# Kernel tuning notes

Hardware: AMD Instinct MI355X
Metric: run time of the kernel (lower is better)

Reference implementation:

```python
import jax, jax.numpy as jnp
import numpy as np

LEVELS = [(64, 64), (32, 32), (16, 16), (8, 8)]  # (H, W) per feature level
B, C, NH, NL, NP, NLAYERS, FFN = 8, 256, 8, 4, 4, 6, 1024
Q = sum(h * w for h, w in LEVELS)  # 5440
DH = C // NH


def setup_inputs() -> dict:
    key = jax.random.key(0)
    ks = iter(jax.random.split(key, 40))
    def rn(shape, s=0.02):
        return jax.random.normal(next(ks), shape, dtype=jnp.float32) * s
    return {
        'src_flat': jax.random.normal(next(ks), (B, Q, C), dtype=jnp.float32),
        'pos_flat': jax.random.normal(next(ks), (B, Q, C), dtype=jnp.float32) * 0.1,
        'level_embed': rn((NL, C), 0.1),
        'W_samp': rn((NLAYERS, C, NH * NL * NP * 2)),
        'b_samp': rn((NLAYERS, NH * NL * NP * 2), 0.1),
        'W_attn': rn((NLAYERS, C, NH * NL * NP)),
        'b_attn': rn((NLAYERS, NH * NL * NP), 0.1),
        'W_val': rn((NLAYERS, C, C)),
        'b_val': jnp.zeros((NLAYERS, C), jnp.float32),
        'W_out': rn((NLAYERS, C, C)),
        'b_out': jnp.zeros((NLAYERS, C), jnp.float32),
        'g1': jnp.ones((NLAYERS, C), jnp.float32),
        'b1': jnp.zeros((NLAYERS, C), jnp.float32),
        'W_fc1': rn((NLAYERS, C, FFN)),
        'b_fc1': jnp.zeros((NLAYERS, FFN), jnp.float32),
        'W_fc2': rn((NLAYERS, FFN, C)),
        'b_fc2': jnp.zeros((NLAYERS, C), jnp.float32),
        'g2': jnp.ones((NLAYERS, C), jnp.float32),
        'b2': jnp.zeros((NLAYERS, C), jnp.float32),
    }


def layer_norm(x, g, b):
    m = x.mean(-1, keepdims=True)
    v = ((x - m) ** 2).mean(-1, keepdims=True)
    return (x - m) * jax.lax.rsqrt(v + 1e-5) * g + b


def get_reference_points():
    # valid_ratios are all ones (masks are all-False), so ref pts are identical per level dim
    pts = []
    for (h, w) in LEVELS:
        ry = (jnp.arange(h, dtype=jnp.float32) + 0.5) / h
        rx = (jnp.arange(w, dtype=jnp.float32) + 0.5) / w
        yy, xx = jnp.meshgrid(ry, rx, indexing='ij')
        pts.append(jnp.stack([xx.ravel(), yy.ravel()], -1))
    return jnp.concatenate(pts, 0)  # [Q, 2] in (x, y)


def ms_deform_attn(query, src, ref_pts, Ws, bs, Wa, ba, Wv, bv, Wo, bo):
    value = (src @ Wv + bv).reshape(B, Q, NH, DH)
    off = (query @ Ws + bs).reshape(B, Q, NH, NL, NP, 2)
    aw = jax.nn.softmax((query @ Wa + ba).reshape(B, Q, NH, NL * NP), axis=-1)
    aw = aw.reshape(B, Q, NH, NL, NP).transpose(0, 2, 1, 3, 4)  # [B,NH,Q,NL,NP]
    normalizer = jnp.array([[w, h] for (h, w) in LEVELS], jnp.float32)  # (x, y) per level
    loc = ref_pts[None, :, None, None, None, :] + off / normalizer[None, None, None, :, None, :]
    out = jnp.zeros((B, NH, Q, DH), jnp.float32)
    start = 0
    for l, (h, w) in enumerate(LEVELS):
        v_l = value[:, start:start + h * w].transpose(0, 2, 1, 3)  # [B,NH,HW,DH]
        start += h * w
        loc_l = loc[:, :, :, l]  # [B,Q,NH,NP,2]
        x = loc_l[..., 0] * w - 0.5  # grid_sample align_corners=False pixel coords
        y = loc_l[..., 1] * h - 0.5
        x0 = jnp.floor(x)
        y0 = jnp.floor(y)
        fx = x - x0
        fy = y - y0
        sampled = jnp.zeros((B, NH, Q, NP, DH), jnp.float32)
        for dy, dx in ((0, 0), (0, 1), (1, 0), (1, 1)):
            cy = y0 + dy
            cx = x0 + dx
            wgt = (fy if dy else 1.0 - fy) * (fx if dx else 1.0 - fx)
            valid = (cy >= 0) & (cy < h) & (cx >= 0) & (cx < w)  # zero padding
            wgt = jnp.where(valid, wgt, 0.0)
            idx = (jnp.clip(cy, 0, h - 1) * w + jnp.clip(cx, 0, w - 1)).astype(jnp.int32)
            idx = idx.transpose(0, 2, 1, 3).reshape(B, NH, Q * NP)
            g = jnp.take_along_axis(v_l, idx[..., None], axis=2).reshape(B, NH, Q, NP, DH)
            sampled = sampled + g * wgt.transpose(0, 2, 1, 3)[..., None]
        out = out + (sampled * aw[:, :, :, l, :, None]).sum(3)
    out = out.transpose(0, 2, 1, 3).reshape(B, Q, C)
    return out @ Wo + bo


def reference(src_flat, pos_flat, level_embed, W_samp, b_samp, W_attn, b_attn, W_val, b_val, W_out, b_out, g1, b1, W_fc1, b_fc1, W_fc2, b_fc2, g2, b2):
    counts = np.array([h * w for h, w in LEVELS])
    lvl_emb = jnp.repeat(level_embed, counts, axis=0, total_repeat_length=Q)  # [Q,C]
    pos = pos_flat + lvl_emb[None]
    ref = get_reference_points()
    out = src_flat
    for i in range(NLAYERS):
        q = out + pos
        attn = ms_deform_attn(q, out, ref, W_samp[i], b_samp[i], W_attn[i], b_attn[i], W_val[i], b_val[i], W_out[i], b_out[i])
        out = layer_norm(out + attn, g1[i], b1[i])
        hid = jax.nn.relu(out @ W_fc1[i] + b_fc1[i]) @ W_fc2[i] + b_fc2[i]
        out = layer_norm(out + hid, g2[i], b2[i])
    return out
```

## Files before the change

kernel.cpp:

```cpp
#include <hip/hip_runtime.h>
#include <hip/hip_bf16.h>

#define NB 8
#define NC 256
#define NH_ 8
#define NLAYERS_ 6
#define FFN_ 1024
#define Q_ 5440
#define DH_ 32
#define M_ (NB*Q_)
#define MC2 (M_/2)

typedef __attribute__((ext_vector_type(8))) short bf16x8;
typedef __attribute__((ext_vector_type(4))) short bf16x4;
typedef __attribute__((ext_vector_type(4))) float f32x4;
typedef __attribute__((ext_vector_type(4))) int i32x4;
typedef __attribute__((ext_vector_type(4))) unsigned int u32x4;
typedef unsigned int u32;
typedef unsigned short ushort_t;

__device__ __forceinline__ unsigned short f2bf(float f) {
  unsigned int u = __float_as_uint(f);
  u += 0x7fffu + ((u >> 16) & 1u);
  return (unsigned short)(u >> 16);
}
__device__ __forceinline__ float bf2f(unsigned short s) {
  return __uint_as_float(((unsigned int)s) << 16);
}
__device__ __forceinline__ void gl16(const unsigned short* g, unsigned short* l) {
  __builtin_amdgcn_global_load_lds((const __attribute__((address_space(1))) u32*)(g),
                                   (__attribute__((address_space(3))) u32*)(l), 16, 0, 0);
}

__global__ void transpose_w2_k(const float* __restrict__ W, unsigned short* __restrict__ Wt,
                               int L, int Kd, int Nd, int NdTot, int nOff) {
  size_t total = (size_t)L * Nd * Kd;
  for (size_t i = (size_t)blockIdx.x * blockDim.x + threadIdx.x; i < total;
       i += (size_t)gridDim.x * blockDim.x) {
    int k = (int)(i % Kd);
    size_t r = i / Kd;
    int n = (int)(r % Nd);
    int l = (int)(r / Nd);
    Wt[((size_t)l * NdTot + nOff + n) * Kd + k] = f2bf(W[((size_t)l * Kd + k) * Nd + n]);
  }
}

__global__ void bias_cat_k(const float* __restrict__ bs, const float* __restrict__ ba,
                           float* __restrict__ bsa) {
  int i = blockIdx.x * blockDim.x + threadIdx.x;
  if (i >= NLAYERS_ * 384) return;
  int l = i / 384, n = i % 384;
  bsa[i] = (n < 256) ? bs[l * 256 + n] : ba[l * 128 + (n - 256)];
}

__global__ __launch_bounds__(256)
void pre_k(const float* __restrict__ src, const float* __restrict__ pf,
           const float* __restrict__ le, unsigned short* __restrict__ xb,
           unsigned short* __restrict__ pe, unsigned short* __restrict__ qb) {
  int row = blockIdx.x * 4 + (threadIdx.x >> 6);
  int lane = threadIdx.x & 63;
  size_t base = (size_t)row * NC + lane * 4;
  int q = row % Q_;
  int lvl = q < 4096 ? 0 : (q < 5120 ? 1 : (q < 5376 ? 2 : 3));
  f32x4 xv = *(const f32x4*)(src + base);
  f32x4 pv = *(const f32x4*)(pf + base) + *(const f32x4*)(le + lvl * NC + lane * 4);
  f32x4 qv = xv + pv;
  bf16x4 xo, po, qo;
#pragma unroll
  for (int j = 0; j < 4; ++j) {
    xo[j] = (short)f2bf(xv[j]); po[j] = (short)f2bf(pv[j]); qo[j] = (short)f2bf(qv[j]);
  }
  *(bf16x4*)(xb + base) = xo;
  *(bf16x4*)(pe + base) = po;
  *(bf16x4*)(qb + base) = qo;
}

__device__ __forceinline__ int swz(int r, int sl) { return sl ^ (r & 3) ^ ((r >> 2) & 3); }
#define ES 136

template <bool RELU>
__device__ __forceinline__ void gemm_body(const unsigned short* X, const unsigned short* Wt,
                                          const float* bias, unsigned short* Y,
                                          int Kdim, int Ndim, int n0, int m0,
                                          unsigned short* SH) {
  unsigned short* A0 = SH;
  unsigned short* B0 = SH + 8192;
  const int t = threadIdx.x;
  const int wave = t >> 6, lane = t & 63;
  const int wr = wave >> 1, wc = wave & 1;
  const int lr = lane & 15, lk = lane >> 4;
  const int r0 = t >> 2, sl0 = t & 3;
  const int r1 = (256 + t) >> 2;
  const int gs0 = swz(r0, sl0);
  const int gs1 = swz(r1, sl0);
  const unsigned short* xp0 = X + (size_t)(m0 + r0) * Kdim + gs0 * 8;
  const unsigned short* wp0 = Wt + (size_t)(n0 + r0) * Kdim + gs0 * 8;
  const unsigned short* xp1 = X + (size_t)(m0 + r1) * Kdim + gs1 * 8;
  const unsigned short* wp1 = Wt + (size_t)(n0 + r1) * Kdim + gs1 * 8;

  f32x4 acc[4][4];
#pragma unroll
  for (int i = 0; i < 4; ++i)
#pragma unroll
    for (int j = 0; j < 4; ++j)
#pragma unroll
      for (int e = 0; e < 4; ++e) acc[i][j][e] = 0.f;

  auto stage = [&](int buf, int kt) {
    gl16(xp0 + kt, A0 + buf * 4096 + t * 8);
    gl16(wp0 + kt, B0 + buf * 4096 + t * 8);
    gl16(xp1 + kt, A0 + buf * 4096 + (256 + t) * 8);
    gl16(wp1 + kt, B0 + buf * 4096 + (256 + t) * 8);
  };

  stage(0, 0);
  __syncthreads();
  const int nt = Kdim >> 5;
  int cur = 0;
  for (int ti = 0; ti < nt; ++ti) {
    if (ti + 1 < nt) stage(cur ^ 1, (ti + 1) << 5);
    bf16x8 ar[4], br[4];
#pragma unroll
    for (int fi = 0; fi < 4; ++fi) {
      int r = wr * 64 + fi * 16 + lr;
      ar[fi] = *(const bf16x8*)&A0[cur * 4096 + r * 32 + swz(r, lk) * 8];
    }
#pragma unroll
    for (int fj = 0; fj < 4; ++fj) {
      int r = wc * 64 + fj * 16 + lr;
      br[fj] = *(const bf16x8*)&B0[cur * 4096 + r * 32 + swz(r, lk) * 8];
    }
#pragma unroll
    for (int fi = 0; fi < 4; ++fi)
#pragma unroll
      for (int fj = 0; fj < 4; ++fj)
        acc[fi][fj] = __builtin_amdgcn_mfma_f32_16x16x32_bf16(ar[fi], br[fj], acc[fi][fj], 0, 0, 0);
    __syncthreads();
    cur ^= 1;
  }

#pragma unroll
  for (int fi = 0; fi < 4; ++fi)
#pragma unroll
    for (int fj = 0; fj < 4; ++fj) {
      int col = wc * 64 + fj * 16 + lr;
      float bv = bias[n0 + col];
#pragma unroll
      for (int rr = 0; rr < 4; ++rr) {
        int row = wr * 64 + fi * 16 + lk * 4 + rr;
        float v = acc[fi][fj][rr] + bv;
        if constexpr (RELU) v = fmaxf(v, 0.f);
        SH[row * ES + col] = f2bf(v);
      }
    }
  __syncthreads();
  {
    int row = t >> 1, hcol = (t & 1) * 64;
    const unsigned short* sp = SH + row * ES + hcol;
    unsigned short* dp = Y + (size_t)(m0 + row) * Ndim + n0 + hcol;
#pragma unroll
    for (int j = 0; j < 8; ++j)
      *(bf16x8*)(dp + j * 8) = *(const bf16x8*)(sp + j * 8);
  }
}

template <bool RELU>
__global__ __launch_bounds__(256)
void gemm_k(const unsigned short* __restrict__ X, const unsigned short* __restrict__ Wt,
            const float* __restrict__ bias, unsigned short* __restrict__ Y,
            int Kdim, int Ndim) {
  __shared__ unsigned short SH[128 * ES];
  gemm_body<RELU>(X, Wt, bias, Y, Kdim, Ndim, blockIdx.x * 128, blockIdx.y * 128, SH);
}

__global__ __launch_bounds__(256)
void gemm_vs_k(const unsigned short* __restrict__ X0, const unsigned short* __restrict__ W0,
               const float* __restrict__ b0, unsigned short* __restrict__ Y0,
               const unsigned short* __restrict__ X1, const unsigned short* __restrict__ W1,
               const float* __restrict__ b1, unsigned short* __restrict__ Y1) {
  __shared__ unsigned short SH[128 * ES];
  int bx = blockIdx.x, m0 = blockIdx.y * 128;
  if (bx < 2)
    gemm_body<false>(X0, W0, b0, Y0, 256, 256, bx * 128, m0, SH);
  else
    gemm_body<false>(X1, W1, b1, Y1, 256, 384, (bx - 2) * 128, m0, SH);
}

__global__ __launch_bounds__(256)
void samp_k(const unsigned short* __restrict__ value, const unsigned short* __restrict__ sa,
            unsigned short* __restrict__ attn_feat) {
  __shared__ float lw[4][128][4];
  __shared__ int   la[4][128][4];
  const int wid = threadIdx.x >> 6, lane = threadIdx.x & 63;
  const int bq = blockIdx.x * 4 + wid;
  const int q = bq % Q_;
  const int b = bq / Q_;

  int lvl = q < 4096 ? 0 : (q < 5120 ? 1 : (q < 5376 ? 2 : 3));
  int qrem = q - (lvl == 0 ? 0 : lvl == 1 ? 4096 : lvl == 2 ? 5120 : 5376);
  int wlog = 6 - lvl;
  float inv = __uint_as_float((unsigned)(127 - wlog) << 23);
  float refx = ((qrem & ((1 << wlog) - 1)) + 0.5f) * inv;
  float refy = ((qrem >> wlog) + 0.5f) * inv;
  const unsigned short* sa_bq = sa + (size_t)bq * 384;

  const int h_s = lane >> 3;
  const int s0 = (lane & 7) * 2;
  unsigned lg01 = *(const unsigned*)&sa_bq[256 + h_s * 16 + s0];
  float lg0 = bf2f((unsigned short)(lg01 & 0xffff));
  float lg1 = bf2f((unsigned short)(lg01 >> 16));
  float mx = fmaxf(lg0, lg1);
  mx = fmaxf(mx, __shfl_xor(mx, 1));
  mx = fmaxf(mx, __shfl_xor(mx, 2));
  mx = fmaxf(mx, __shfl_xor(mx, 4));
  float e0 = __expf(lg0 - mx), e1 = __expf(lg1 - mx);
  float sm = e0 + e1;
  sm += __shfl_xor(sm, 1);
  sm += __shfl_xor(sm, 2);
  sm += __shfl_xor(sm, 4);
  float rs = 1.0f / sm;

#pragma unroll
  for (int j = 0; j < 2; ++j) {
    int s = s0 + j;
    float aw = (j ? e1 : e0) * rs;
    unsigned oxy = *(const unsigned*)&sa_bq[h_s * 32 + s * 2];
    float ox = bf2f((unsigned short)(oxy & 0xffff));
    float oy = bf2f((unsigned short)(oxy >> 16));
    int sl = s >> 2;
    int swl = 6 - sl;
    int sw = 1 << swl;
    int sstart = (sl == 0) ? 0 : (sl == 1) ? 4096 : (sl == 2) ? 5120 : 5376;
    float x = fmaf(refx, (float)sw, ox) - 0.5f;
    float y = fmaf(refy, (float)sw, oy) - 0.5f;
    float x0f = floorf(x), y0f = floorf(y);
    float fx = x - x0f, fy = y - y0f;
    int x0 = (int)x0f, y0 = (int)y0f;
    int rowbase = b * Q_ + sstart;
    f32x4 wv; i32x4 av;
#pragma unroll
    for (int c = 0; c < 4; ++c) {
      int dy = c >> 1, dx = c & 1;
      int cy = y0 + dy, cx = x0 + dx;
      float wgt = (dy ? fy : 1.f - fy) * (dx ? fx : 1.f - fx);
      bool valid = (cy >= 0) & (cy < sw) & (cx >= 0) & (cx < sw);
      wgt = valid ? wgt : 0.f;
      int ccy = min(max(cy, 0), sw - 1);
      int ccx = min(max(cx, 0), sw - 1);
      wv[c] = wgt * aw;
      av[c] = ((rowbase + (ccy << swl) + ccx) * NH_ + h_s) * DH_;
    }
    int idx = s * 8 + (h_s ^ (s & 7));
    *(f32x4*)&lw[wid][idx][0] = wv;
    *(i32x4*)&la[wid][idx][0] = av;
  }
  __syncthreads();

  const int h = lane >> 3;
  const int half = (lane >> 2) & 1;
  const int quad = lane & 3;
  const unsigned short* vq = value + quad * 8;
  f32x4 accA = {0.f, 0.f, 0.f, 0.f}, accB = {0.f, 0.f, 0.f, 0.f};
#pragma unroll
  for (int i = 0; i < 8; ++i) {
    int s = half * 8 + i;
    int idx = s * 8 + (h ^ (s & 7));
    f32x4 wv = *(const f32x4*)&lw[wid][idx][0];
    i32x4 av = *(const i32x4*)&la[wid][idx][0];
#pragma unroll
    for (int c = 0; c < 4; ++c) {
      u32x4 g = *(const u32x4*)(vq + av[c]);
      f32x4 v0, v1;
      v0[0] = __uint_as_float(g[0] << 16); v0[1] = __uint_as_float(g[0] & 0xffff0000u);
      v0[2] = __uint_as_float(g[1] << 16); v0[3] = __uint_as_float(g[1] & 0xffff0000u);
      v1[0] = __uint_as_float(g[2] << 16); v1[1] = __uint_as_float(g[2] & 0xffff0000u);
      v1[2] = __uint_as_float(g[3] << 16); v1[3] = __uint_as_float(g[3] & 0xffff0000u);
      float wcc = wv[c];
      accA += v0 * wcc;
      accB += v1 * wcc;
    }
  }
#pragma unroll
  for (int j = 0; j < 4; ++j) {
    accA[j] += __shfl_xor(accA[j], 4);
    accB[j] += __shfl_xor(accB[j], 4);
  }
  if (half == 0) {
    bf16x8 ov;
    ov[0] = (short)f2bf(accA[0]); ov[1] = (short)f2bf(accA[1]);
    ov[2] = (short)f2bf(accA[2]); ov[3] = (short)f2bf(accA[3]);
    ov[4] = (short)f2bf(accB[0]); ov[5] = (short)f2bf(accB[1]);
    ov[6] = (short)f2bf(accB[2]); ov[7] = (short)f2bf(accB[3]);
    *(bf16x8*)(attn_feat + (size_t)bq * NC + h * DH_ + quad * 8) = ov;
  }
}

__device__ __forceinline__ f32x4 ln_core(f32x4 xv, const float* g, const float* bta, int lane) {
  float ssum = xv[0] + xv[1] + xv[2] + xv[3];
#pragma unroll
  for (int o = 1; o <= 32; o <<= 1) ssum += __shfl_xor(ssum, o);
  float mean = ssum * (1.0f / NC);
  f32x4 cv = xv - mean;
  float s2 = cv[0] * cv[0] + cv[1] * cv[1] + cv[2] * cv[2] + cv[3] * cv[3];
#pragma unroll
  for (int o = 1; o <= 32; o <<= 1) s2 += __shfl_xor(s2, o);
  float rstd = rsqrtf(s2 * (1.0f / NC) + 1e-5f);
  f32x4 gv = *(const f32x4*)(g + lane * 4);
  f32x4 bv = *(const f32x4*)(bta + lane * 4);
  return cv * rstd * gv + bv;
}
__device__ __forceinline__ f32x4 ldbf4(const unsigned short* p) {
  bf16x4 v = *(const bf16x4*)p;
  f32x4 r;
#pragma unroll
  for (int j = 0; j < 4; ++j) r[j] = bf2f((unsigned short)v[j]);
  return r;
}
__device__ __forceinline__ void stbf4(unsigned short* p, f32x4 v) {
  bf16x4 o;
#pragma unroll
  for (int j = 0; j < 4; ++j) o[j] = (short)f2bf(v[j]);
  *(bf16x4*)p = o;
}

__global__ __launch_bounds__(256)
void ln_mid_k(const unsigned short* __restrict__ xb, const unsigned short* __restrict__ delta,
              const float* __restrict__ g, const float* __restrict__ bta,
              unsigned short* __restrict__ xm) {
  int row = blockIdx.x * 4 + (threadIdx.x >> 6);
  int lane = threadIdx.x & 63;
  size_t base = (size_t)row * NC + lane * 4;
  f32x4 xv = ldbf4(xb + base) + ldbf4(delta + base);
  f32x4 ov = ln_core(xv, g, bta, lane);
  stbf4(xm + base, ov);
}

template <bool FINAL>
__global__ __launch_bounds__(256)
void ln_end_k(const unsigned short* __restrict__ xm, const unsigned short* __restrict__ delta,
              const float* __restrict__ g, const float* __restrict__ bta,
              const unsigned short* __restrict__ pe,
              unsigned short* __restrict__ xb, unsigned short* __restrict__ qb,
              float* __restrict__ outf) {
  int row = blockIdx.x * 4 + (threadIdx.x >> 6);
  int lane = threadIdx.x & 63;
  size_t base = (size_t)row * NC + lane * 4;
  f32x4 xv = ldbf4(xm + base) + ldbf4(delta + base);
  f32x4 ov = ln_core(xv, g, bta, lane);
  stbf4(xb + base, ov);
  f32x4 qv = ov + ldbf4(pe + base);
  stbf4(qb + base, qv);
  if constexpr (FINAL) *(f32x4*)(outf + base) = ov;
}

extern "C" void kernel_launch(void* const* d_in, const int* in_sizes, int n_in,
                              void* d_out, int out_size, void* d_ws, size_t ws_size,
                              hipStream_t stream) {
  const float* src      = (const float*)d_in[0];
  const float* pos_flat = (const float*)d_in[1];
  const float* lvl_emb  = (const float*)d_in[2];
  const float* W_samp   = (const float*)d_in[3];
  const float* b_samp   = (const float*)d_in[4];
  const float* W_attn   = (const float*)d_in[5];
  const float* b_attn   = (const float*)d_in[6];
  const float* W_val    = (const float*)d_in[7];
  const float* b_val    = (const float*)d_in[8];
  const float* W_out    = (const float*)d_in[9];
  const float* b_out    = (const float*)d_in[10];
  const float* g1       = (const float*)d_in[11];
  const float* b1       = (const float*)d_in[12];
  const float* W_fc1    = (const float*)d_in[13];
  const float* b_fc1    = (const float*)d_in[14];
  const float* W_fc2    = (const float*)d_in[15];
  const float* b_fc2    = (const float*)d_in[16];
  const float* g2       = (const float*)d_in[17];
  const float* b2       = (const float*)d_in[18];

  char* ws = (char*)d_ws;
  size_t o = 0;
  auto alloc = [&](size_t bytes) {
    void* p = ws + o;
    o += (bytes + 255) & ~(size_t)255;
    return p;
  };
  unsigned short* bb    = (unsigned short*)alloc((size_t)MC2 * FFN_ * 2);
  unsigned short* sa    = (unsigned short*)alloc((size_t)M_ * 384 * 2);
  unsigned short* af    = (unsigned short*)alloc((size_t)M_ * NC * 2);
  unsigned short* xb    = (unsigned short*)alloc((size_t)M_ * NC * 2);
  unsigned short* xm    = (unsigned short*)alloc((size_t)M_ * NC * 2);
  unsigned short* qb    = (unsigned short*)alloc((size_t)M_ * NC * 2);
  unsigned short* pe    = (unsigned short*)alloc((size_t)M_ * NC * 2);
  unsigned short* Wv_t  = (unsigned short*)alloc((size_t)6 * 256 * 256 * 2);
  unsigned short* Wsa_t = (unsigned short*)alloc((size_t)6 * 384 * 256 * 2);
  unsigned short* Wo_t  = (unsigned short*)alloc((size_t)6 * 256 * 256 * 2);
  unsigned short* Wf1_t = (unsigned short*)alloc((size_t)6 * 1024 * 256 * 2);
  unsigned short* Wf2_t = (unsigned short*)alloc((size_t)6 * 256 * 1024 * 2);
  float* bsa            = (float*)alloc((size_t)6 * 384 * 4);

  transpose_w2_k<<<1536, 256, 0, stream>>>(W_val, Wv_t, 6, 256, 256, 256, 0);
  transpose_w2_k<<<1536, 256, 0, stream>>>(W_samp, Wsa_t, 6, 256, 256, 384, 0);
  transpose_w2_k<<<768, 256, 0, stream>>>(W_attn, Wsa_t, 6, 256, 128, 384, 256);
  transpose_w2_k<<<1536, 256, 0, stream>>>(W_out, Wo_t, 6, 256, 256, 256, 0);
  transpose_w2_k<<<3072, 256, 0, stream>>>(W_fc1, Wf1_t, 6, 256, 1024, 1024, 0);
  transpose_w2_k<<<3072, 256, 0, stream>>>(W_fc2, Wf2_t, 6, 1024, 256, 256, 0);
  bias_cat_k<<<9, 256, 0, stream>>>(b_samp, b_attn, bsa);
  pre_k<<<M_ / 4, 256, 0, stream>>>(src, pos_flat, lvl_emb, xb, pe, qb);

  for (int i = 0; i < NLAYERS_; ++i) {
    gemm_vs_k<<<dim3(5, M_ / 128), 256, 0, stream>>>(
        xb, Wv_t + (size_t)i * 65536, b_val + i * 256, bb,
        qb, Wsa_t + (size_t)i * 98304, bsa + i * 384, sa);
    samp_k<<<M_ / 4, 256, 0, stream>>>(bb, sa, af);
    gemm_k<false><<<dim3(2, M_ / 128), 256, 0, stream>>>(
        af, Wo_t + (size_t)i * 65536, b_out + i * 256, sa, 256, 256);
    ln_mid_k<<<M_ / 4, 256, 0, stream>>>(xb, sa, g1 + i * 256, b1 + i * 256, xm);
    for (int c = 0; c < 2; ++c) {
      gemm_k<true><<<dim3(8, MC2 / 128), 256, 0, stream>>>(
          xm + (size_t)c * MC2 * NC, Wf1_t + (size_t)i * 262144, b_fc1 + i * 1024, bb, 256, 1024);
      gemm_k<false><<<dim3(2, MC2 / 128), 256, 0, stream>>>(
          bb, Wf2_t + (size_t)i * 262144, b_fc2 + i * 256, sa + (size_t)c * MC2 * NC, 1024, 256);
    }
    if (i == NLAYERS_ - 1)
      ln_end_k<true><<<M_ / 4, 256, 0, stream>>>(xm, sa, g2 + i * 256, b2 + i * 256,
                                                 pe, xb, qb, (float*)d_out);
    else
      ln_end_k<false><<<M_ / 4, 256, 0, stream>>>(xm, sa, g2 + i * 256, b2 + i * 256,
                                                  pe, xb, qb, nullptr);
  }
}
```

Before: 1.698 ms.

## Triple-buffer GEMM LDS staging with explicit vmcnt waits and raw barriers

Converts the GEMM main loop from double to triple buffering in LDS: two k-tiles are prefetched up front, and each iteration issues the load for tile ti+2. The full __syncthreads is replaced by s_waitcnt vmcnt(4) plus s_barrier, so one tile's loads stay in flight across the barrier. The aim is to hide global-to-LDS latency behind the MFMA work. The cost is more LDS per block (48KB instead of about 34KB), which may reduce occupancy.

```diff
diff --git a/kernel.cpp b/kernel.cpp
--- a/kernel.cpp
+++ b/kernel.cpp
@@ -17,7 +17,6 @@
 typedef __attribute__((ext_vector_type(4))) int i32x4;
 typedef __attribute__((ext_vector_type(4))) unsigned int u32x4;
 typedef unsigned int u32;
-typedef unsigned short ushort_t;
 
 __device__ __forceinline__ unsigned short f2bf(float f) {
   unsigned int u = __float_as_uint(f);
@@ -77,14 +76,13 @@
 
 __device__ __forceinline__ int swz(int r, int sl) { return sl ^ (r & 3) ^ ((r >> 2) & 3); }
 #define ES 136
+#define SHN 24576
 
 template <bool RELU>
 __device__ __forceinline__ void gemm_body(const unsigned short* X, const unsigned short* Wt,
                                           const float* bias, unsigned short* Y,
                                           int Kdim, int Ndim, int n0, int m0,
                                           unsigned short* SH) {
-  unsigned short* A0 = SH;
-  unsigned short* B0 = SH + 8192;
   const int t = threadIdx.x;
   const int wave = t >> 6, lane = t & 63;
   const int wr = wave >> 1, wc = wave & 1;
@@ -107,36 +105,46 @@
       for (int e = 0; e < 4; ++e) acc[i][j][e] = 0.f;
 
   auto stage = [&](int buf, int kt) {
-    gl16(xp0 + kt, A0 + buf * 4096 + t * 8);
-    gl16(wp0 + kt, B0 + buf * 4096 + t * 8);
-    gl16(xp1 + kt, A0 + buf * 4096 + (256 + t) * 8);
-    gl16(wp1 + kt, B0 + buf * 4096 + (256 + t) * 8);
+    unsigned short* base = SH + buf * 8192;
+    gl16(xp0 + kt, base + t * 8);
+    gl16(wp0 + kt, base + 4096 + t * 8);
+    gl16(xp1 + kt, base + (256 + t) * 8);
+    gl16(wp1 + kt, base + 4096 + (256 + t) * 8);
   };
 
+  const int nt = Kdim >> 5;
   stage(0, 0);
-  __syncthreads();
-  const int nt = Kdim >> 5;
-  int cur = 0;
+  stage(1, 32);
+  asm volatile("s_waitcnt vmcnt(4)" ::: "memory");
+  __builtin_amdgcn_s_barrier();
+
+  int buf = 0;
   for (int ti = 0; ti < nt; ++ti) {
-    if (ti + 1 < nt) stage(cur ^ 1, (ti + 1) << 5);
+    if (ti + 2 < nt) stage(buf == 0 ? 2 : buf - 1, (ti + 2) << 5);
+    const unsigned short* Ab = SH + buf * 8192;
+    const unsigned short* Bb = Ab + 4096;
     bf16x8 ar[4], br[4];
 #pragma unroll
     for (int fi = 0; fi < 4; ++fi) {
       int r = wr * 64 + fi * 16 + lr;
-      ar[fi] = *(const bf16x8*)&A0[cur * 4096 + r * 32 + swz(r, lk) * 8];
+      ar[fi] = *(const bf16x8*)&Ab[r * 32 + swz(r, lk) * 8];
     }
 #pragma unroll
     for (int fj = 0; fj < 4; ++fj) {
       int r = wc * 64 + fj * 16 + lr;
-      br[fj] = *(const bf16x8*)&B0[cur * 4096 + r * 32 + swz(r, lk) * 8];
+      br[fj] = *(const bf16x8*)&Bb[r * 32 + swz(r, lk) * 8];
     }
 #pragma unroll
     for (int fi = 0; fi < 4; ++fi)
 #pragma unroll
       for (int fj = 0; fj < 4; ++fj)
         acc[fi][fj] = __builtin_amdgcn_mfma_f32_16x16x32_bf16(ar[fi], br[fj], acc[fi][fj], 0, 0, 0);
-    __syncthreads();
-    cur ^= 1;
+    if (ti + 2 < nt)
+      asm volatile("s_waitcnt vmcnt(4)" ::: "memory");
+    else
+      asm volatile("s_waitcnt vmcnt(0)" ::: "memory");
+    __builtin_amdgcn_s_barrier();
+    buf = (buf == 2) ? 0 : buf + 1;
   }
 
 #pragma unroll
@@ -169,7 +177,7 @@
 void gemm_k(const unsigned short* __restrict__ X, const unsigned short* __restrict__ Wt,
             const float* __restrict__ bias, unsigned short* __restrict__ Y,
             int Kdim, int Ndim) {
-  __shared__ unsigned short SH[128 * ES];
+  __shared__ unsigned short SH[SHN];
   gemm_body<RELU>(X, Wt, bias, Y, Kdim, Ndim, blockIdx.x * 128, blockIdx.y * 128, SH);
 }
 
@@ -178,7 +186,7 @@
                const float* __restrict__ b0, unsigned short* __restrict__ Y0,
                const unsigned short* __restrict__ X1, const unsigned short* __restrict__ W1,
                const float* __restrict__ b1, unsigned short* __restrict__ Y1) {
-  __shared__ unsigned short SH[128 * ES];
+  __shared__ unsigned short SH[SHN];
   int bx = blockIdx.x, m0 = blockIdx.y * 128;
   if (bx < 2)
     gemm_body<false>(X0, W0, b0, Y0, 256, 256, bx * 128, m0, SH);
```

Result: faster. 1.660 ms (-2.2%).
